# Optimization experiments

Hardware: AMD Instinct MI355X
Metric: run time of the kernel (lower is better)

## Reference

```python
import jax, jax.numpy as jnp
import numpy as np

N_NODES = 50000
N_EDGES = 800000
N_GRAPHS = 128
HIDDEN = 64
HEADS = 2
OUT = 4
NEG_SLOPE = 0.2
ALPHA_FLAG = 0.05


def _gat_conv(x, src, dst, W, a_src, a_dst, b):
    # PyG GATConv, concat=False (mean over heads), self-loops already appended.
    N = x.shape[0]
    H, C = a_src.shape
    xh = (x @ W).reshape(N, H, C)                       # [N,H,C]
    s_src = (xh * a_src).sum(-1)                        # [N,H]
    s_dst = (xh * a_dst).sum(-1)                        # [N,H]
    e = s_src[src] + s_dst[dst]                         # [E,H]
    e = jnp.where(e > 0, e, NEG_SLOPE * e)              # LeakyReLU(0.2)
    emax = jax.ops.segment_max(e, dst, num_segments=N)  # per-dst softmax max
    emax = jnp.where(jnp.isfinite(emax), emax, 0.0)
    p = jnp.exp(e - emax[dst])
    denom = jax.ops.segment_sum(p, dst, num_segments=N)
    alpha = p / (denom[dst] + 1e-16)                    # [E,H]
    out = jax.ops.segment_sum(alpha[:, :, None] * xh[src], dst, num_segments=N)
    return out.mean(axis=1) + b                         # [N,HIDDEN]


def setup_inputs() -> dict:
    key = jax.random.key(0)
    ks = jax.random.split(key, 32)
    f = lambda k, shape, s=0.1: (jax.random.normal(k, shape) * s).astype(jnp.float32)
    inp = {}
    inp['x_all'] = jax.random.normal(ks[0], (N_NODES, 8), dtype=jnp.float32)
    inp['climber'] = jax.random.normal(ks[1], (N_GRAPHS, 4), dtype=jnp.float32)
    inp['edge_index'] = jax.random.randint(ks[2], (2, N_EDGES), 0, N_NODES)
    inp['batch'] = jnp.sort(jax.random.randint(ks[3], (N_NODES,), 0, N_GRAPHS))
    H = HIDDEN
    inp['W_in'] = f(ks[4], (6, H)); inp['b_in'] = jnp.zeros((H,), jnp.float32)
    inp['W_c'] = f(ks[5], (4, H)); inp['b_c'] = jnp.zeros((H,), jnp.float32)
    inp['W_f1'] = f(ks[6], (H, 2 * H)); inp['b_f1'] = jnp.zeros((2 * H,), jnp.float32)
    inp['W_f2'] = f(ks[7], (H, 2 * H)); inp['b_f2'] = jnp.zeros((2 * H,), jnp.float32)
    inp['W_g1'] = f(ks[8], (H, HEADS * H)); inp['a_src1'] = f(ks[9], (HEADS, H)); inp['a_dst1'] = f(ks[10], (HEADS, H)); inp['b_g1'] = jnp.zeros((H,), jnp.float32)
    inp['W_g2'] = f(ks[11], (H, HEADS * H)); inp['a_src2'] = f(ks[12], (HEADS, H)); inp['a_dst2'] = f(ks[13], (HEADS, H)); inp['b_g2'] = jnp.zeros((H,), jnp.float32)
    inp['W_cl1'] = f(ks[14], (H, H)); inp['b_cl1'] = jnp.zeros((H,), jnp.float32)
    inp['W_cl2'] = f(ks[15], (H, OUT)); inp['b_cl2'] = jnp.zeros((OUT,), jnp.float32)
    inp['W_fh1'] = f(ks[16], (2, 8), 0.001); inp['b_fh1'] = jnp.zeros((8,), jnp.float32)
    inp['W_fh2'] = f(ks[17], (8, OUT), 0.001); inp['b_fh2'] = jnp.zeros((OUT,), jnp.float32)
    return inp


def reference(x_all, climber, edge_index, batch, W_in, b_in, W_c, b_c,
              W_f1, b_f1, W_f2, b_f2,
              W_g1, a_src1, a_dst1, b_g1,
              W_g2, a_src2, a_dst2, b_g2,
              W_cl1, b_cl1, W_cl2, b_cl2,
              W_fh1, b_fh1, W_fh2, b_fh2):
    N = x_all.shape[0]
    flags = x_all[:, -2:]
    x = x_all[:, :-2]
    # climber embedding (eval mode -> dropout is identity)
    c = jax.nn.relu(climber @ W_c + b_c)                 # [G,H]
    x = x @ W_in + b_in                                  # [N,H]
    # FiLM 1
    gb = c @ W_f1 + b_f1
    gamma, beta = jnp.split(gb, 2, axis=-1)
    x = x * (1.0 + gamma[batch]) + beta[batch]
    # add self-loops (PyG GATConv default)
    loop = jnp.arange(N, dtype=edge_index.dtype)
    src = jnp.concatenate([edge_index[0], loop])
    dst = jnp.concatenate([edge_index[1], loop])
    x = jax.nn.relu(_gat_conv(x, src, dst, W_g1, a_src1, a_dst1, b_g1))
    # FiLM 2
    gb = c @ W_f2 + b_f2
    gamma, beta = jnp.split(gb, 2, axis=-1)
    x = x * (1.0 + gamma[batch]) + beta[batch]
    x = jax.nn.relu(_gat_conv(x, src, dst, W_g2, a_src2, a_dst2, b_g2))
    logits_main = jax.nn.relu(x @ W_cl1 + b_cl1) @ W_cl2 + b_cl2
    logits_flag = jax.nn.relu(flags @ W_fh1 + b_fh1) @ W_fh2 + b_fh2
    return logits_main + ALPHA_FLAG * logits_flag
```

## Files before the change

kernel.cpp:

```cpp
#include <hip/hip_runtime.h>
#include <hip/hip_fp16.h>

#define NEG_SLOPE 0.2f
#define ALPHA_FLAG 0.05f

typedef _Float16 h2t __attribute__((ext_vector_type(2)));
union h2u { unsigned u; h2t h; __half2 hh; float f; };
static __device__ __forceinline__ h2t u_as_h2(unsigned u) { h2u c; c.u = u; return c.h; }
static __device__ __forceinline__ float h2_as_f(__half2 h) { h2u c; c.hh = h; return c.f; }
static __device__ __forceinline__ h2t f_as_h2(float f) { h2u c; c.f = f; return c.h; }

static inline size_t align256(size_t x) { return (x + 255) & ~(size_t)255; }

__global__ void prep_kernel(const float* __restrict__ climber,
                            const float* __restrict__ W_c, const float* __restrict__ b_c,
                            const float* __restrict__ W_f1, const float* __restrict__ b_f1,
                            const float* __restrict__ W_f2, const float* __restrict__ b_f2,
                            float* __restrict__ gb1, float* __restrict__ gb2) {
    __shared__ float c_sh[64];
    int g = blockIdx.x, t = threadIdx.x;
    if (t < 64) {
        float acc = b_c[t];
#pragma unroll
        for (int k = 0; k < 4; ++k) acc = fmaf(climber[g * 4 + k], W_c[k * 64 + t], acc);
        c_sh[t] = fmaxf(acc, 0.f);
    }
    __syncthreads();
    float a1 = b_f1[t], a2 = b_f2[t];
#pragma unroll 8
    for (int h = 0; h < 64; ++h) {
        float cv = c_sh[h];
        a1 = fmaf(cv, W_f1[h * 128 + t], a1);
        a2 = fmaf(cv, W_f2[h * 128 + t], a2);
    }
    gb1[g * 128 + t] = a1;
    gb2[g * 128 + t] = a2;
}

__global__ void hist_kernel(const int* __restrict__ dst, int E,
                            int* __restrict__ counts, int* __restrict__ ranks) {
    int i4 = (blockIdx.x * blockDim.x + threadIdx.x) * 4;
    if (i4 + 3 < E) {
        int4 d = *(const int4*)&dst[i4];
        int4 r;
        r.x = atomicAdd(&counts[d.x], 1);
        r.y = atomicAdd(&counts[d.y], 1);
        r.z = atomicAdd(&counts[d.z], 1);
        r.w = atomicAdd(&counts[d.w], 1);
        *(int4*)&ranks[i4] = r;
    } else {
        for (int u = 0; u < 4; ++u)
            if (i4 + u < E) ranks[i4 + u] = atomicAdd(&counts[dst[i4 + u]], 1);
    }
}

#define SCAN_CHUNK 1024
__global__ void scan_kernel(const int* __restrict__ counts, int* __restrict__ row_ptr, int N) {
    __shared__ int sh[256];
    int b = blockIdx.x, t = threadIdx.x;
    int pre = 0;
    for (int i0 = t * 4; i0 < b * SCAN_CHUNK; i0 += 1024) {
        int4 v = *(const int4*)&counts[i0];
        pre += v.x + v.y + v.z + v.w + 4;
    }
    sh[t] = pre;
    __syncthreads();
#pragma unroll
    for (int off = 128; off; off >>= 1) {
        if (t < off) sh[t] += sh[t + off];
        __syncthreads();
    }
    int base = sh[0];
    __syncthreads();
    int idx0 = b * SCAN_CHUNK + t * 4;
    int c[4];
    if (idx0 + 3 < N) {
        int4 v = *(const int4*)&counts[idx0];
        c[0] = v.x + 1; c[1] = v.y + 1; c[2] = v.z + 1; c[3] = v.w + 1;
    } else {
#pragma unroll
        for (int u = 0; u < 4; ++u) c[u] = (idx0 + u < N) ? counts[idx0 + u] + 1 : 0;
    }
    int s = c[0] + c[1] + c[2] + c[3];
    sh[t] = s;
    __syncthreads();
#pragma unroll
    for (int off = 1; off < 256; off <<= 1) {
        int add = (t >= off) ? sh[t - off] : 0;
        __syncthreads();
        sh[t] += add;
        __syncthreads();
    }
    int run = base + sh[t] - s;
#pragma unroll
    for (int u = 0; u < 4; ++u) {
        if (idx0 + u < N) {
            row_ptr[idx0 + u] = run;
            run += c[u];
            if (idx0 + u == N - 1) row_ptr[N] = run;
        }
    }
}

__global__ void scatter_kernel(const int* __restrict__ src, const int* __restrict__ dst,
                               const int* __restrict__ ranks, const int* __restrict__ counts,
                               const int* __restrict__ row_ptr,
                               int Eh, int N, int* __restrict__ csr_src) {
    int t = blockIdx.x * blockDim.x + threadIdx.x;
    if (t < Eh) {
        int2 s2 = *(const int2*)&src[t * 2];
        int2 d2 = *(const int2*)&dst[t * 2];
        int2 r2 = *(const int2*)&ranks[t * 2];
        csr_src[row_ptr[d2.x] + r2.x] = s2.x;
        csr_src[row_ptr[d2.y] + r2.y] = s2.y;
    } else {
        int i = t - Eh;
        if (i < N) csr_src[row_ptr[i] + counts[i]] = i;
    }
}

#define XH_NB 32
__global__ __launch_bounds__(256, 4) void xh_kernel(
    const __half* __restrict__ xhalf, const float* __restrict__ W_g,
    const float* __restrict__ a_src, const float* __restrict__ a_dst,
    __half* __restrict__ xh, float* __restrict__ s_src, float* __restrict__ s_dst,
    int N, int in_mode,
    const float* __restrict__ x_all, const int* __restrict__ batch,
    const float* __restrict__ W_in, const float* __restrict__ b_in,
    const float* __restrict__ gb1) {
    __shared__ float x_sh[XH_NB * 64];
    __shared__ float win_sh[6 * 64 + 64];
    int t = threadIdx.x;
    int base = blockIdx.x * XH_NB;
    if (in_mode) {
        for (int i = t; i < 448; i += 256)
            win_sh[i] = (i < 384) ? W_in[i] : b_in[i - 384];
        __syncthreads();
        int nd = t >> 3;
        int jb = (t & 7) * 8;
        int n = base + nd;
        if (n < N) {
            float4 a = *(const float4*)&x_all[(size_t)n * 8];
            float2 b = *(const float2*)&x_all[(size_t)n * 8 + 4];
            float xa[6] = {a.x, a.y, a.z, a.w, b.x, b.y};
            int g = batch[n];
            const float* gbrow = &gb1[g * 128];
#pragma unroll
            for (int jj = 0; jj < 8; ++jj) {
                int j = jb + jj;
                float acc = win_sh[384 + j];
#pragma unroll
                for (int k = 0; k < 6; ++k) acc = fmaf(xa[k], win_sh[k * 64 + j], acc);
                x_sh[nd * 64 + j] = acc * (1.f + gbrow[j]) + gbrow[64 + j];
            }
        } else {
#pragma unroll
            for (int jj = 0; jj < 8; ++jj) x_sh[nd * 64 + jb + jj] = 0.f;
        }
    } else {
        int nvalid = N - base; if (nvalid > XH_NB) nvalid = XH_NB;
        int nhalves = nvalid * 64;
        int idx = t * 8;
        uint4 raw = make_uint4(0, 0, 0, 0);
        if (idx < nhalves) raw = *(const uint4*)&xhalf[(size_t)base * 64 + idx];
        float2 f0 = __half22float2(*(__half2*)&raw.x);
        float2 f1 = __half22float2(*(__half2*)&raw.y);
        float2 f2 = __half22float2(*(__half2*)&raw.z);
        float2 f3 = __half22float2(*(__half2*)&raw.w);
        x_sh[idx + 0] = f0.x; x_sh[idx + 1] = f0.y;
        x_sh[idx + 2] = f1.x; x_sh[idx + 3] = f1.y;
        x_sh[idx + 4] = f2.x; x_sh[idx + 5] = f2.y;
        x_sh[idx + 6] = f3.x; x_sh[idx + 7] = f3.y;
    }
    __syncthreads();
    int c = t & 63;
    int g = t >> 6;
    float acc0[8], acc1[8];
#pragma unroll
    for (int i = 0; i < 8; ++i) { acc0[i] = 0.f; acc1[i] = 0.f; }
    const float* W0 = W_g + c;
    const float* W1 = W_g + 64 + c;
#pragma unroll 2
    for (int k = 0; k < 64; k += 4) {
        float w0[4], w1[4];
#pragma unroll
        for (int u = 0; u < 4; ++u) { w0[u] = W0[(k + u) * 128]; w1[u] = W1[(k + u) * 128]; }
#pragma unroll
        for (int i = 0; i < 8; ++i) {
            float4 xv = *(const float4*)&x_sh[(g * 8 + i) * 64 + k];
            acc0[i] = fmaf(xv.x, w0[0], acc0[i]);
            acc0[i] = fmaf(xv.y, w0[1], acc0[i]);
            acc0[i] = fmaf(xv.z, w0[2], acc0[i]);
            acc0[i] = fmaf(xv.w, w0[3], acc0[i]);
            acc1[i] = fmaf(xv.x, w1[0], acc1[i]);
            acc1[i] = fmaf(xv.y, w1[1], acc1[i]);
            acc1[i] = fmaf(xv.z, w1[2], acc1[i]);
            acc1[i] = fmaf(xv.w, w1[3], acc1[i]);
        }
    }
    float as0 = a_src[c], ad0 = a_dst[c];
    float as1 = a_src[64 + c], ad1 = a_dst[64 + c];
#pragma unroll
    for (int i = 0; i < 8; ++i) {
        int n = base + g * 8 + i;
        float ps0 = acc0[i] * as0, pd0 = acc0[i] * ad0;
        float ps1 = acc1[i] * as1, pd1 = acc1[i] * ad1;
#pragma unroll
        for (int off = 32; off; off >>= 1) {
            ps0 += __shfl_xor(ps0, off); pd0 += __shfl_xor(pd0, off);
            ps1 += __shfl_xor(ps1, off); pd1 += __shfl_xor(pd1, off);
        }
        if (n < N) {
            if (c == 0) {
                s_src[n * 2 + 0] = ps0; s_src[n * 2 + 1] = ps1;
                s_dst[n * 2 + 0] = pd0; s_dst[n * 2 + 1] = pd1;
            }
            __half2 hv = __floats2half2_rn(acc0[i], acc1[i]);
            *(__half2*)&xh[(size_t)n * 128 + c * 2] = hv;
        }
    }
}

static __device__ __forceinline__ float dot2acc(unsigned xbits, h2t w, float acc) {
#if __has_builtin(__builtin_amdgcn_fdot2)
    return __builtin_amdgcn_fdot2(u_as_h2(xbits), w, acc, false);
#else
    h2u cx; cx.u = xbits;
    float2 xf = __half22float2(cx.hh);
    h2u cw; cw.h = w;
    float2 wf = __half22float2(cw.hh);
    return fmaf(xf.x, wf.x, fmaf(xf.y, wf.y, acc));
#endif
}

static __device__ __forceinline__ void agg_one_slow(
    const char* __restrict__ xhb, const float* __restrict__ s_src,
    float2 sd, const int* __restrict__ csr_src, int beg, int end,
    int lane, int sub, unsigned q16, float2* __restrict__ ps_slot,
    float acc[4]) {
    float dp0 = 0.f, dp1 = 0.f;
    for (int chunk = beg; chunk < end; chunk += 64) {
        int m = end - chunk; if (m > 64) m = 64;
        if (lane < m) {
            int s = csr_src[chunk + lane];
            float2 ss = *(const float2*)&s_src[s * 2];
            float e0 = ss.x + sd.x, e1 = ss.y + sd.y;
            e0 = (e0 > 0.f) ? e0 : NEG_SLOPE * e0;
            e1 = (e1 > 0.f) ? e1 : NEG_SLOPE * e1;
            dp0 += __expf(e0); dp1 += __expf(e1);
        }
    }
#pragma unroll
    for (int off = 32; off; off >>= 1) {
        dp0 += __shfl_xor(dp0, off);
        dp1 += __shfl_xor(dp1, off);
    }
    float i0 = 0.5f / (dp0 + 1e-16f), i1 = 0.5f / (dp1 + 1e-16f);
    for (int chunk = beg; chunk < end; chunk += 64) {
        int m = end - chunk; if (m > 64) m = 64;
        float p0 = 0.f, p1 = 0.f; unsigned sb = 0;
        if (lane < m) {
            int s = csr_src[chunk + lane];
            sb = (unsigned)s << 8;
            float2 ss = *(const float2*)&s_src[s * 2];
            float e0 = ss.x + sd.x, e1 = ss.y + sd.y;
            e0 = (e0 > 0.f) ? e0 : NEG_SLOPE * e0;
            e1 = (e1 > 0.f) ? e1 : NEG_SLOPE * e1;
            p0 = __expf(e0); p1 = __expf(e1);
        }
        ps_slot[lane] = make_float2(h2_as_f(__floats2half2_rn(p0 * i0, p1 * i1)),
                                    __uint_as_float(sb));
        int mr = (m + 3) & ~3;
#pragma unroll 4
        for (int j = 0; j < mr; j += 4) {
            float2 ps = ps_slot[j + sub];
            h2t wpk = f_as_h2(ps.x);
            unsigned voff = __float_as_uint(ps.y) + q16;
            uint4 hv = *(const uint4*)(xhb + voff);
            acc[0] = dot2acc(hv.x, wpk, acc[0]);
            acc[1] = dot2acc(hv.y, wpk, acc[1]);
            acc[2] = dot2acc(hv.z, wpk, acc[2]);
            acc[3] = dot2acc(hv.w, wpk, acc[3]);
        }
    }
}

template <int MODE>
static __device__ __forceinline__ void agg_impl(
    const __half* __restrict__ xh, const float* __restrict__ s_src,
    const float* __restrict__ s_dst, const int* __restrict__ row_ptr,
    const int* __restrict__ csr_src, const float* __restrict__ b_g,
    const int* __restrict__ batch, const float* __restrict__ gb_film,
    __half* __restrict__ xout_h, int N, int half,
    const float* __restrict__ x_all,
    const float* __restrict__ W_cl1, const float* __restrict__ b_cl1,
    const float* __restrict__ W_cl2, const float* __restrict__ b_cl2,
    const float* __restrict__ W_fh1, const float* __restrict__ b_fh1,
    const float* __restrict__ W_fh2, const float* __restrict__ b_fh2,
    float* __restrict__ out) {
    __shared__ float2 ps_sh[4][2][64];
    __shared__ float vh_sh[4][2][64];
    int lane = threadIdx.x & 63;
    int w = threadIdx.x >> 6;
    int n0 = (blockIdx.x * blockDim.x + threadIdx.x) >> 6;
    if (n0 >= half) return;
    int n1 = n0 + half;
    bool valid1 = n1 < N;
    const char* xhb = (const char*)xh;
    int sub = lane >> 4;
    unsigned q16 = (unsigned)(lane & 15) * 16u;
    float accA[4] = {0.f, 0.f, 0.f, 0.f};
    float accB[4] = {0.f, 0.f, 0.f, 0.f};

    int begA = row_ptr[n0], endA = row_ptr[n0 + 1];
    int begB = valid1 ? row_ptr[n1] : 0, endB = valid1 ? row_ptr[n1 + 1] : 0;
    int degA = endA - begA, degB = endB - begB;
    float2 sdA = *(const float2*)&s_dst[n0 * 2];
    float2 sdB = valid1 ? *(const float2*)&s_dst[n1 * 2] : make_float2(0.f, 0.f);

    if (degA <= 64 && degB <= 64) {
        int sA = (lane < degA) ? csr_src[begA + lane] : -1;
        int sB = (lane < degB) ? csr_src[begB + lane] : -1;
        float2 ssA = (sA >= 0) ? *(const float2*)&s_src[sA * 2] : make_float2(0.f, 0.f);
        float2 ssB = (sB >= 0) ? *(const float2*)&s_src[sB * 2] : make_float2(0.f, 0.f);
        float pA0 = 0.f, pA1 = 0.f, pB0 = 0.f, pB1 = 0.f;
        unsigned sbA = 0, sbB = 0;
        if (sA >= 0) {
            sbA = (unsigned)sA << 8;
            float e0 = ssA.x + sdA.x, e1 = ssA.y + sdA.y;
            e0 = (e0 > 0.f) ? e0 : NEG_SLOPE * e0;
            e1 = (e1 > 0.f) ? e1 : NEG_SLOPE * e1;
            pA0 = __expf(e0); pA1 = __expf(e1);
        }
        if (sB >= 0) {
            sbB = (unsigned)sB << 8;
            float e0 = ssB.x + sdB.x, e1 = ssB.y + sdB.y;
            e0 = (e0 > 0.f) ? e0 : NEG_SLOPE * e0;
            e1 = (e1 > 0.f) ? e1 : NEG_SLOPE * e1;
            pB0 = __expf(e0); pB1 = __expf(e1);
        }
        float dA0 = pA0, dA1 = pA1, dB0 = pB0, dB1 = pB1;
#pragma unroll
        for (int off = 32; off; off >>= 1) {
            dA0 += __shfl_xor(dA0, off); dA1 += __shfl_xor(dA1, off);
            dB0 += __shfl_xor(dB0, off); dB1 += __shfl_xor(dB1, off);
        }
        float iA0 = 0.5f / (dA0 + 1e-16f), iA1 = 0.5f / (dA1 + 1e-16f);
        float iB0 = 0.5f / (dB0 + 1e-16f), iB1 = 0.5f / (dB1 + 1e-16f);
        ps_sh[w][0][lane] = make_float2(h2_as_f(__floats2half2_rn(pA0 * iA0, pA1 * iA1)),
                                        __uint_as_float(sbA));
        ps_sh[w][1][lane] = make_float2(h2_as_f(__floats2half2_rn(pB0 * iB0, pB1 * iB1)),
                                        __uint_as_float(sbB));
        int mrA = (degA + 3) & ~3, mrB = (degB + 3) & ~3;
        int mr = mrA > mrB ? mrA : mrB;
#pragma unroll 2
        for (int j = 0; j < mr; j += 4) {
            float2 psA = ps_sh[w][0][j + sub];
            float2 psB = ps_sh[w][1][j + sub];
            unsigned voA = __float_as_uint(psA.y) + q16;
            unsigned voB = __float_as_uint(psB.y) + q16;
            uint4 hvA = *(const uint4*)(xhb + voA);
            uint4 hvB = *(const uint4*)(xhb + voB);
            h2t wA = f_as_h2(psA.x), wB = f_as_h2(psB.x);
            accA[0] = dot2acc(hvA.x, wA, accA[0]);
            accA[1] = dot2acc(hvA.y, wA, accA[1]);
            accA[2] = dot2acc(hvA.z, wA, accA[2]);
            accA[3] = dot2acc(hvA.w, wA, accA[3]);
            accB[0] = dot2acc(hvB.x, wB, accB[0]);
            accB[1] = dot2acc(hvB.y, wB, accB[1]);
            accB[2] = dot2acc(hvB.z, wB, accB[2]);
            accB[3] = dot2acc(hvB.w, wB, accB[3]);
        }
    } else {
        agg_one_slow(xhb, s_src, sdA, csr_src, begA, endA, lane, sub, q16,
                     &ps_sh[w][0][0], accA);
        if (valid1)
            agg_one_slow(xhb, s_src, sdB, csr_src, begB, endB, lane, sub, q16,
                         &ps_sh[w][1][0], accB);
    }
#pragma unroll
    for (int u = 0; u < 4; ++u) {
        accA[u] += __shfl_xor(accA[u], 16);
        accA[u] += __shfl_xor(accA[u], 32);
        accB[u] += __shfl_xor(accB[u], 16);
        accB[u] += __shfl_xor(accB[u], 32);
    }
    if (lane < 16) {
        *(float4*)&vh_sh[w][0][lane * 4] = make_float4(accA[0], accA[1], accA[2], accA[3]);
        *(float4*)&vh_sh[w][1][lane * 4] = make_float4(accB[0], accB[1], accB[2], accB[3]);
    }
    float bg = b_g[lane];
    float vA = fmaxf(vh_sh[w][0][lane] + bg, 0.f);
    float vB = fmaxf(vh_sh[w][1][lane] + bg, 0.f);
    if (MODE == 0) {
        int gA = batch[n0];
        vA = vA * (1.f + gb_film[gA * 128 + lane]) + gb_film[gA * 128 + 64 + lane];
        xout_h[(size_t)n0 * 64 + lane] = __float2half(vA);
        if (valid1) {
            int gB = batch[n1];
            vB = vB * (1.f + gb_film[gB * 128 + lane]) + gb_film[gB * 128 + 64 + lane];
            xout_h[(size_t)n1 * 64 + lane] = __float2half(vB);
        }
        return;
    }
    vh_sh[w][0][lane] = vA;
    vh_sh[w][1][lane] = vB;
    float4 w2 = *(const float4*)&W_cl2[lane * 4];
    float b1v = b_cl1[lane];
    for (int q = 0; q < 2; ++q) {
        int n = q ? n1 : n0;
        if (q && !valid1) break;
        float h = b1v;
#pragma unroll 4
        for (int k = 0; k < 64; k += 4) {
            float4 vq = *(const float4*)&vh_sh[w][q][k];
            h = fmaf(vq.x, W_cl1[(k + 0) * 64 + lane], h);
            h = fmaf(vq.y, W_cl1[(k + 1) * 64 + lane], h);
            h = fmaf(vq.z, W_cl1[(k + 2) * 64 + lane], h);
            h = fmaf(vq.w, W_cl1[(k + 3) * 64 + lane], h);
        }
        h = fmaxf(h, 0.f);
        float o0 = h * w2.x, o1 = h * w2.y, o2 = h * w2.z, o3 = h * w2.w;
#pragma unroll
        for (int off = 32; off; off >>= 1) {
            o0 += __shfl_xor(o0, off); o1 += __shfl_xor(o1, off);
            o2 += __shfl_xor(o2, off); o3 += __shfl_xor(o3, off);
        }
        if (lane < 4) {
            float f0 = x_all[(size_t)n * 8 + 6], f1 = x_all[(size_t)n * 8 + 7];
            float lf = b_fh2[lane];
#pragma unroll
            for (int m = 0; m < 8; ++m) {
                float fm = fmaxf(fmaf(f0, W_fh1[m], fmaf(f1, W_fh1[8 + m], b_fh1[m])), 0.f);
                lf = fmaf(fm, W_fh2[m * 4 + lane], lf);
            }
            float om = (lane == 0) ? o0 : (lane == 1) ? o1 : (lane == 2) ? o2 : o3;
            out[(size_t)n * 4 + lane] = om + b_cl2[lane] + ALPHA_FLAG * lf;
        }
    }
}

__global__ __launch_bounds__(256) void agg_film_kernel(
    const __half* xh, const float* s_src, const float* s_dst, const int* row_ptr,
    const int* csr_src, const float* b_g, const int* batch, const float* gb_film,
    __half* xout_h, int N, int half) {
    agg_impl<0>(xh, s_src, s_dst, row_ptr, csr_src, b_g, batch, gb_film, xout_h, N, half,
                nullptr, nullptr, nullptr, nullptr, nullptr, nullptr, nullptr,
                nullptr, nullptr, nullptr);
}

__global__ __launch_bounds__(256) void agg_cls_kernel(
    const __half* xh, const float* s_src, const float* s_dst, const int* row_ptr,
    const int* csr_src, const float* b_g, int N, int half, const float* x_all,
    const float* W_cl1, const float* b_cl1, const float* W_cl2, const float* b_cl2,
    const float* W_fh1, const float* b_fh1, const float* W_fh2, const float* b_fh2,
    float* out) {
    agg_impl<1>(xh, s_src, s_dst, row_ptr, csr_src, b_g, nullptr, nullptr, nullptr, N, half,
                x_all, W_cl1, b_cl1, W_cl2, b_cl2, W_fh1, b_fh1, W_fh2, b_fh2, out);
}

extern "C" void kernel_launch(void* const* d_in, const int* in_sizes, int n_in,
                              void* d_out, int out_size, void* d_ws, size_t ws_size,
                              hipStream_t stream) {
    const float* x_all   = (const float*)d_in[0];
    const float* climber = (const float*)d_in[1];
    const int*   eidx    = (const int*)d_in[2];
    const int*   batch   = (const int*)d_in[3];
    const float* W_in  = (const float*)d_in[4];
    const float* b_in  = (const float*)d_in[5];
    const float* W_c   = (const float*)d_in[6];
    const float* b_c   = (const float*)d_in[7];
    const float* W_f1  = (const float*)d_in[8];
    const float* b_f1  = (const float*)d_in[9];
    const float* W_f2  = (const float*)d_in[10];
    const float* b_f2  = (const float*)d_in[11];
    const float* W_g1  = (const float*)d_in[12];
    const float* a_s1  = (const float*)d_in[13];
    const float* a_d1  = (const float*)d_in[14];
    const float* b_g1  = (const float*)d_in[15];
    const float* W_g2  = (const float*)d_in[16];
    const float* a_s2  = (const float*)d_in[17];
    const float* a_d2  = (const float*)d_in[18];
    const float* b_g2  = (const float*)d_in[19];
    const float* W_cl1 = (const float*)d_in[20];
    const float* b_cl1 = (const float*)d_in[21];
    const float* W_cl2 = (const float*)d_in[22];
    const float* b_cl2 = (const float*)d_in[23];
    const float* W_fh1 = (const float*)d_in[24];
    const float* b_fh1 = (const float*)d_in[25];
    const float* W_fh2 = (const float*)d_in[26];
    const float* b_fh2 = (const float*)d_in[27];
    float* out = (float*)d_out;

    const int N = in_sizes[0] / 8;
    const int E = in_sizes[2] / 2;
    const int G = in_sizes[1] / 4;
    const int* src = eidx;
    const int* dst = eidx + E;
    const int NB_SCAN = (N + SCAN_CHUNK - 1) / SCAN_CHUNK;
    const int half = (N + 1) / 2;

    char* ws = (char*)d_ws;
    size_t off = 0;
    auto alloc = [&](size_t bytes) { char* p = ws + off; off += align256(bytes); return p; };
    float*  gb1     = (float*)alloc((size_t)G * 128 * 4);
    float*  gb2     = (float*)alloc((size_t)G * 128 * 4);
    __half* xbuf    = (__half*)alloc((size_t)N * 64 * 2);
    __half* xh      = (__half*)alloc((size_t)N * 128 * 2);
    float*  s_src   = (float*)alloc((size_t)N * 2 * 4);
    float*  s_dst   = (float*)alloc((size_t)N * 2 * 4);
    int*    counts  = (int*)alloc((size_t)N * 4);
    int*    ranks   = (int*)alloc((size_t)E * 4);
    int*    row_ptr = (int*)alloc((size_t)(N + 1) * 4);
    int*    csr_src = (int*)alloc((size_t)(E + N) * 4);
    (void)ws_size;

    prep_kernel<<<G, 128, 0, stream>>>(climber, W_c, b_c, W_f1, b_f1, W_f2, b_f2, gb1, gb2);
    hipMemsetAsync(counts, 0, (size_t)N * 4, stream);
    hist_kernel<<<(E / 4 + 255) / 256, 256, 0, stream>>>(dst, E, counts, ranks);
    scan_kernel<<<NB_SCAN, 256, 0, stream>>>(counts, row_ptr, N);
    scatter_kernel<<<(E / 2 + N + 255) / 256, 256, 0, stream>>>(src, dst, ranks, counts,
                                                                row_ptr, E / 2, N, csr_src);
    xh_kernel<<<(N + XH_NB - 1) / XH_NB, 256, 0, stream>>>(nullptr, W_g1, a_s1, a_d1, xh,
                                                           s_src, s_dst, N, 1,
                                                           x_all, batch, W_in, b_in, gb1);
    agg_film_kernel<<<(half * 64 + 255) / 256, 256, 0, stream>>>(xh, s_src, s_dst, row_ptr,
                                                                 csr_src, b_g1, batch, gb2,
                                                                 xbuf, N, half);
    xh_kernel<<<(N + XH_NB - 1) / XH_NB, 256, 0, stream>>>(xbuf, W_g2, a_s2, a_d2, xh,
                                                           s_src, s_dst, N, 0,
                                                           nullptr, nullptr, nullptr, nullptr, nullptr);
    agg_cls_kernel<<<(half * 64 + 255) / 256, 256, 0, stream>>>(xh, s_src, s_dst, row_ptr,
                                                                csr_src, b_g2, N, half, x_all,
                                                                W_cl1, b_cl1, W_cl2, b_cl2,
                                                                W_fh1, b_fh1, W_fh2, b_fh2, out);
}
```

Measured before the change: 220.7 us.

## Merge prep with histogram and scatter with first projection into combined launches

```diff
diff --git a/kernel.cpp b/kernel.cpp
--- a/kernel.cpp
+++ b/kernel.cpp
@@ -12,34 +12,39 @@
 
 static inline size_t align256(size_t x) { return (x + 255) & ~(size_t)255; }
 
-__global__ void prep_kernel(const float* __restrict__ climber,
-                            const float* __restrict__ W_c, const float* __restrict__ b_c,
-                            const float* __restrict__ W_f1, const float* __restrict__ b_f1,
-                            const float* __restrict__ W_f2, const float* __restrict__ b_f2,
-                            float* __restrict__ gb1, float* __restrict__ gb2) {
+__global__ __launch_bounds__(256) void prep_hist_kernel(
+    const float* __restrict__ climber,
+    const float* __restrict__ W_c, const float* __restrict__ b_c,
+    const float* __restrict__ W_f1, const float* __restrict__ b_f1,
+    const float* __restrict__ W_f2, const float* __restrict__ b_f2,
+    float* __restrict__ gb1, float* __restrict__ gb2, int G,
+    const int* __restrict__ dst, int E,
+    int* __restrict__ counts, int* __restrict__ ranks) {
     __shared__ float c_sh[64];
-    int g = blockIdx.x, t = threadIdx.x;
-    if (t < 64) {
-        float acc = b_c[t];
-#pragma unroll
-        for (int k = 0; k < 4; ++k) acc = fmaf(climber[g * 4 + k], W_c[k * 64 + t], acc);
-        c_sh[t] = fmaxf(acc, 0.f);
-    }
-    __syncthreads();
-    float a1 = b_f1[t], a2 = b_f2[t];
+    int t = threadIdx.x;
+    if ((int)blockIdx.x < G) {
+        int g = blockIdx.x;
+        if (t < 64) {
+            float acc = b_c[t];
+#pragma unroll
+            for (int k = 0; k < 4; ++k) acc = fmaf(climber[g * 4 + k], W_c[k * 64 + t], acc);
+            c_sh[t] = fmaxf(acc, 0.f);
+        }
+        __syncthreads();
+        if (t < 128) {
+            float a1 = b_f1[t], a2 = b_f2[t];
 #pragma unroll 8
-    for (int h = 0; h < 64; ++h) {
-        float cv = c_sh[h];
-        a1 = fmaf(cv, W_f1[h * 128 + t], a1);
-        a2 = fmaf(cv, W_f2[h * 128 + t], a2);
-    }
-    gb1[g * 128 + t] = a1;
-    gb2[g * 128 + t] = a2;
-}
-
-__global__ void hist_kernel(const int* __restrict__ dst, int E,
-                            int* __restrict__ counts, int* __restrict__ ranks) {
-    int i4 = (blockIdx.x * blockDim.x + threadIdx.x) * 4;
+            for (int h = 0; h < 64; ++h) {
+                float cv = c_sh[h];
+                a1 = fmaf(cv, W_f1[h * 128 + t], a1);
+                a2 = fmaf(cv, W_f2[h * 128 + t], a2);
+            }
+            gb1[g * 128 + t] = a1;
+            gb2[g * 128 + t] = a2;
+        }
+        return;
+    }
+    int i4 = ((blockIdx.x - G) * 256 + t) * 4;
     if (i4 + 3 < E) {
         int4 d = *(const int4*)&dst[i4];
         int4 r;
@@ -102,37 +107,17 @@
     }
 }
 
-__global__ void scatter_kernel(const int* __restrict__ src, const int* __restrict__ dst,
-                               const int* __restrict__ ranks, const int* __restrict__ counts,
-                               const int* __restrict__ row_ptr,
-                               int Eh, int N, int* __restrict__ csr_src) {
-    int t = blockIdx.x * blockDim.x + threadIdx.x;
-    if (t < Eh) {
-        int2 s2 = *(const int2*)&src[t * 2];
-        int2 d2 = *(const int2*)&dst[t * 2];
-        int2 r2 = *(const int2*)&ranks[t * 2];
-        csr_src[row_ptr[d2.x] + r2.x] = s2.x;
-        csr_src[row_ptr[d2.y] + r2.y] = s2.y;
-    } else {
-        int i = t - Eh;
-        if (i < N) csr_src[row_ptr[i] + counts[i]] = i;
-    }
-}
-
 #define XH_NB 32
-__global__ __launch_bounds__(256, 4) void xh_kernel(
-    const __half* __restrict__ xhalf, const float* __restrict__ W_g,
+template <int IN_MODE>
+static __device__ __forceinline__ void xh_body(
+    int base, const __half* __restrict__ xhalf, const float* __restrict__ W_g,
     const float* __restrict__ a_src, const float* __restrict__ a_dst,
     __half* __restrict__ xh, float* __restrict__ s_src, float* __restrict__ s_dst,
-    int N, int in_mode,
-    const float* __restrict__ x_all, const int* __restrict__ batch,
+    int N, const float* __restrict__ x_all, const int* __restrict__ batch,
     const float* __restrict__ W_in, const float* __restrict__ b_in,
-    const float* __restrict__ gb1) {
-    __shared__ float x_sh[XH_NB * 64];
-    __shared__ float win_sh[6 * 64 + 64];
+    const float* __restrict__ gb1, float* __restrict__ x_sh, float* __restrict__ win_sh) {
     int t = threadIdx.x;
-    int base = blockIdx.x * XH_NB;
-    if (in_mode) {
+    if (IN_MODE) {
         for (int i = t; i < 448; i += 256)
             win_sh[i] = (i < 384) ? W_in[i] : b_in[i - 384];
         __syncthreads();
@@ -219,6 +204,48 @@
             *(__half2*)&xh[(size_t)n * 128 + c * 2] = hv;
         }
     }
+}
+
+__global__ __launch_bounds__(256) void scatter_xh1_kernel(
+    const int* __restrict__ src, const int* __restrict__ dst,
+    const int* __restrict__ ranks, const int* __restrict__ counts,
+    const int* __restrict__ row_ptr, int Eh, int N, int NBS,
+    int* __restrict__ csr_src,
+    const float* __restrict__ W_g, const float* __restrict__ a_src,
+    const float* __restrict__ a_dst, __half* __restrict__ xh,
+    float* __restrict__ s_src, float* __restrict__ s_dst,
+    const float* __restrict__ x_all, const int* __restrict__ batch,
+    const float* __restrict__ W_in, const float* __restrict__ b_in,
+    const float* __restrict__ gb1) {
+    __shared__ float x_sh[XH_NB * 64];
+    __shared__ float win_sh[6 * 64 + 64];
+    if ((int)blockIdx.x < NBS) {
+        int t = blockIdx.x * 256 + threadIdx.x;
+        if (t < Eh) {
+            int2 s2 = *(const int2*)&src[t * 2];
+            int2 d2 = *(const int2*)&dst[t * 2];
+            int2 r2 = *(const int2*)&ranks[t * 2];
+            csr_src[row_ptr[d2.x] + r2.x] = s2.x;
+            csr_src[row_ptr[d2.y] + r2.y] = s2.y;
+        } else {
+            int i = t - Eh;
+            if (i < N) csr_src[row_ptr[i] + counts[i]] = i;
+        }
+        return;
+    }
+    int base = (blockIdx.x - NBS) * XH_NB;
+    xh_body<1>(base, nullptr, W_g, a_src, a_dst, xh, s_src, s_dst, N,
+               x_all, batch, W_in, b_in, gb1, x_sh, win_sh);
+}
+
+__global__ __launch_bounds__(256, 4) void xh2_kernel(
+    const __half* __restrict__ xhalf, const float* __restrict__ W_g,
+    const float* __restrict__ a_src, const float* __restrict__ a_dst,
+    __half* __restrict__ xh, float* __restrict__ s_src, float* __restrict__ s_dst, int N) {
+    __shared__ float x_sh[XH_NB * 64];
+    __shared__ float win_sh[6 * 64 + 64];
+    xh_body<0>(blockIdx.x * XH_NB, xhalf, W_g, a_src, a_dst, xh, s_src, s_dst, N,
+               nullptr, nullptr, nullptr, nullptr, nullptr, x_sh, win_sh);
 }
 
 static __device__ __forceinline__ float dot2acc(unsigned xbits, h2t w, float acc) {
@@ -498,6 +525,9 @@
     const int* src = eidx;
     const int* dst = eidx + E;
     const int NB_SCAN = (N + SCAN_CHUNK - 1) / SCAN_CHUNK;
+    const int NB_HIST = (E / 4 + 255) / 256;
+    const int NB_SCAT = (E / 2 + N + 255) / 256;
+    const int NB_XH   = (N + XH_NB - 1) / XH_NB;
     const int half = (N + 1) / 2;
 
     char* ws = (char*)d_ws;
@@ -515,21 +545,19 @@
     int*    csr_src = (int*)alloc((size_t)(E + N) * 4);
     (void)ws_size;
 
-    prep_kernel<<<G, 128, 0, stream>>>(climber, W_c, b_c, W_f1, b_f1, W_f2, b_f2, gb1, gb2);
     hipMemsetAsync(counts, 0, (size_t)N * 4, stream);
-    hist_kernel<<<(E / 4 + 255) / 256, 256, 0, stream>>>(dst, E, counts, ranks);
+    prep_hist_kernel<<<G + NB_HIST, 256, 0, stream>>>(climber, W_c, b_c, W_f1, b_f1,
+                                                      W_f2, b_f2, gb1, gb2, G,
+                                                      dst, E, counts, ranks);
     scan_kernel<<<NB_SCAN, 256, 0, stream>>>(counts, row_ptr, N);
-    scatter_kernel<<<(E / 2 + N + 255) / 256, 256, 0, stream>>>(src, dst, ranks, counts,
-                                                                row_ptr, E / 2, N, csr_src);
-    xh_kernel<<<(N + XH_NB - 1) / XH_NB, 256, 0, stream>>>(nullptr, W_g1, a_s1, a_d1, xh,
-                                                           s_src, s_dst, N, 1,
-                                                           x_all, batch, W_in, b_in, gb1);
+    scatter_xh1_kernel<<<NB_SCAT + NB_XH, 256, 0, stream>>>(src, dst, ranks, counts, row_ptr,
+                                                            E / 2, N, NB_SCAT, csr_src,
+                                                            W_g1, a_s1, a_d1, xh, s_src, s_dst,
+                                                            x_all, batch, W_in, b_in, gb1);
     agg_film_kernel<<<(half * 64 + 255) / 256, 256, 0, stream>>>(xh, s_src, s_dst, row_ptr,
                                                                  csr_src, b_g1, batch, gb2,
                                                                  xbuf, N, half);
-    xh_kernel<<<(N + XH_NB - 1) / XH_NB, 256, 0, stream>>>(xbuf, W_g2, a_s2, a_d2, xh,
-                                                           s_src, s_dst, N, 0,
-                                                           nullptr, nullptr, nullptr, nullptr, nullptr);
+    xh2_kernel<<<NB_XH, 256, 0, stream>>>(xbuf, W_g2, a_s2, a_d2, xh, s_src, s_dst, N);
     agg_cls_kernel<<<(half * 64 + 255) / 256, 256, 0, stream>>>(xh, s_src, s_dst, row_ptr,
                                                                 csr_src, b_g2, N, half, x_all,
                                                                 W_cl1, b_cl1, W_cl2, b_cl2,
```

After: 213.8 us. 1.03x faster.
